# Kernel tuning notes

Hardware: AMD Instinct MI355X
Metric: run time of the kernel (lower is better)

Reference implementation:

```python
import jax, jax.numpy as jnp
import numpy as np


def setup_inputs() -> dict:
    key = jax.random.key(0)
    k1, k2 = jax.random.split(key)
    D = 512
    B, N = 32, 512
    panel_embeddings = jax.random.normal(k1, (B, N, D), dtype=jnp.float32)
    # nn.Bilinear(D, D, 1) weight: (1, D, D) -> squeeze to (D, D); bias: scalar
    bound = 1.0 / np.sqrt(D)
    W = jax.random.uniform(k2, (D, D), dtype=jnp.float32, minval=-bound, maxval=bound)
    b = jnp.float32(0.0)
    return {"panel_embeddings": panel_embeddings, "W": W, "b": b}


def reference(panel_embeddings, W, b):
    # score[b,i,j] = x_i^T W x_j + b, with diagonal forced to 0 (loop skips i==j)
    xw = jnp.einsum('bid,de->bie', panel_embeddings, W)          # (B, N, D)
    scores = jnp.einsum('bie,bje->bij', xw, panel_embeddings) + b  # (B, N, N)
    N = panel_embeddings.shape[1]
    mask = ~jnp.eye(N, dtype=bool)
    return jnp.where(mask, scores, jnp.zeros_like(scores))
```

## Files before the change

### kernel.cpp

```cpp
#include <hip/hip_runtime.h>
#include <stdint.h>

#define BATCH 32
#define NDIM 512
#define DDIM 512
#define XELEMS (BATCH * NDIM * DDIM)
#define WELEMS (DDIM * DDIM)

typedef _Float16 f16x8 __attribute__((ext_vector_type(8)));
typedef _Float16 f16x4v __attribute__((ext_vector_type(4)));
typedef float f32x4 __attribute__((ext_vector_type(4)));

__device__ __forceinline__ void gl_lds16(const _Float16* g, _Float16* l) {
    __builtin_amdgcn_global_load_lds(
        (const __attribute__((address_space(1))) unsigned int*)(g),
        (__attribute__((address_space(3))) unsigned int*)(l),
        16, 0, 0);
}

__global__ __launch_bounds__(256) void prep(const float4* __restrict__ X4,
                                            f16x4v* __restrict__ Xh4,
                                            const float* __restrict__ W,
                                            _Float16* __restrict__ Wt) {
    __shared__ float tile[32][33];
    int bid = blockIdx.x;
    if (bid < XELEMS / 4 / 256) {
        int i = bid * 256 + threadIdx.x;
        float4 v = X4[i];
        f16x4v o;
        o.x = (_Float16)v.x;
        o.y = (_Float16)v.y;
        o.z = (_Float16)v.z;
        o.w = (_Float16)v.w;
        Xh4[i] = o;
    } else {
        int t = bid - XELEMS / 4 / 256;
        int bx = t & 15;
        int by = t >> 4;
        int tx = threadIdx.x & 31;
        int ty = threadIdx.x >> 5;
        for (int r = ty; r < 32; r += 8)
            tile[r][tx] = W[(by * 32 + r) * DDIM + bx * 32 + tx];
        __syncthreads();
        for (int r = ty; r < 32; r += 8)
            Wt[(size_t)(bx * 32 + r) * DDIM + by * 32 + tx] = (_Float16)tile[tx][r];
    }
}

__global__ __launch_bounds__(512) void fused(const _Float16* __restrict__ Xh,
                                             const _Float16* __restrict__ Wt,
                                             float* __restrict__ Sout,
                                             const float* __restrict__ bias_ptr) {
    __shared__ __align__(16) _Float16 Ylds[64 * 512];
    __shared__ __align__(16) _Float16 As[8 * 512];
    __shared__ __align__(16) _Float16 Bs[64 * 512];

    const int tid  = threadIdx.x;
    const int lane = tid & 63;
    const int wv   = tid >> 6;
    const int quad = lane >> 4;
    const int l16  = lane & 15;

    const int lr = lane >> 3;
    const int lc = lane & 7;
    const int lk = (lc ^ lr) * 8;

    const int blk   = blockIdx.x;
    const int batch = blk & 31;
    const int r0    = (blk >> 5) * 64;

    const _Float16* Xb = Xh + (size_t)batch * (NDIM * DDIM);

    f32x4 acc[4][4];
#pragma unroll
    for (int i = 0; i < 4; ++i)
#pragma unroll
        for (int j = 0; j < 4; ++j)
            acc[i][j] = (f32x4){0.f, 0.f, 0.f, 0.f};

    for (int it = 0; it < 8; ++it) {
        const int k0 = it * 64;
        gl_lds16(Xb + (size_t)(r0 + wv * 8 + lr) * DDIM + k0 + lk, &As[wv * 512]);
#pragma unroll
        for (int t = 0; t < 8; ++t)
            gl_lds16(Wt + (size_t)(wv * 64 + t * 8 + lr) * DDIM + k0 + lk,
                     &Bs[(wv * 8 + t) * 512]);
        __syncthreads();

#pragma unroll
        for (int kkc = 0; kkc < 8; kkc += 4) {
            const int pa = (((kkc + quad) ^ (l16 & 7)) * 8);
            f16x8 a[4], b[4];
#pragma unroll
            for (int mt = 0; mt < 4; ++mt)
                a[mt] = *(const f16x8*)&As[(mt * 16 + l16) * 64 + pa];
#pragma unroll
            for (int nt = 0; nt < 4; ++nt)
                b[nt] = *(const f16x8*)&Bs[(wv * 64 + nt * 16 + l16) * 64 + pa];
#pragma unroll
            for (int mt = 0; mt < 4; ++mt)
#pragma unroll
                for (int nt = 0; nt < 4; ++nt)
                    acc[mt][nt] = __builtin_amdgcn_mfma_f32_16x16x32_f16(
                        a[mt], b[nt], acc[mt][nt], 0, 0, 0);
        }
        __syncthreads();
    }

#pragma unroll
    for (int mt = 0; mt < 4; ++mt)
#pragma unroll
        for (int nt = 0; nt < 4; ++nt)
#pragma unroll
            for (int r = 0; r < 4; ++r) {
                int i = mt * 16 + quad * 4 + r;
                int e = wv * 64 + nt * 16 + l16;
                int c = e >> 3, j = e & 7;
                Ylds[i * 512 + (((c ^ (i & 7)) << 3) | j)] = (_Float16)acc[mt][nt][r];
            }
    __syncthreads();

#pragma unroll
    for (int i = 0; i < 4; ++i)
#pragma unroll
        for (int j = 0; j < 4; ++j)
            acc[i][j] = (f32x4){0.f, 0.f, 0.f, 0.f};

    for (int it = 0; it < 8; ++it) {
        const int e0 = it * 64;
#pragma unroll
        for (int t = 0; t < 8; ++t)
            gl_lds16(Xb + (size_t)(wv * 64 + t * 8 + lr) * DDIM + e0 + lk,
                     &Bs[(wv * 8 + t) * 512]);
        __syncthreads();

#pragma unroll
        for (int kkc = 0; kkc < 8; kkc += 4) {
            const int pa = (((kkc + quad) ^ (l16 & 7)) * 8);
            const int cy = it * 8 + kkc + quad;
            const int pay = ((cy ^ (l16 & 7)) * 8);
            f16x8 a[4], b[4];
#pragma unroll
            for (int mt = 0; mt < 4; ++mt)
                a[mt] = *(const f16x8*)&Ylds[(mt * 16 + l16) * 512 + pay];
#pragma unroll
            for (int nt = 0; nt < 4; ++nt)
                b[nt] = *(const f16x8*)&Bs[(wv * 64 + nt * 16 + l16) * 64 + pa];
#pragma unroll
            for (int mt = 0; mt < 4; ++mt)
#pragma unroll
                for (int nt = 0; nt < 4; ++nt)
                    acc[mt][nt] = __builtin_amdgcn_mfma_f32_16x16x32_f16(
                        a[mt], b[nt], acc[mt][nt], 0, 0, 0);
        }
        __syncthreads();
    }

    const float bias = bias_ptr[0];
#pragma unroll
    for (int mt = 0; mt < 4; ++mt)
#pragma unroll
        for (int nt = 0; nt < 4; ++nt)
#pragma unroll
            for (int r = 0; r < 4; ++r) {
                int gi = r0 + mt * 16 + quad * 4 + r;
                int gj = wv * 64 + nt * 16 + l16;
                float v = acc[mt][nt][r] + bias;
                if (gi == gj) v = 0.f;
                Sout[((size_t)batch * NDIM + gi) * NDIM + gj] = v;
            }
}

extern "C" void kernel_launch(void* const* d_in, const int* in_sizes, int n_in,
                              void* d_out, int out_size, void* d_ws, size_t ws_size,
                              hipStream_t stream) {
    const float* X  = (const float*)d_in[0];
    const float* W  = (const float*)d_in[1];
    const float* bp = (const float*)d_in[2];
    float* out = (float*)d_out;

    _Float16* Xh = (_Float16*)d_ws;
    _Float16* Wt = Xh + XELEMS;

    prep<<<XELEMS / 4 / 256 + 256, 256, 0, stream>>>((const float4*)X, (f16x4v*)Xh, W, Wt);

    fused<<<256, 512, 0, stream>>>(Xh, Wt, out, bp);

    (void)in_sizes; (void)n_in; (void)out_size; (void)ws_size;
}
```

Baseline: 114.4 us.

## Double-buffer LDS tiles with K=32 steps to overlap global loads and MFMA

Replaces the single-buffered 64-wide K tiles with two 32-wide LDS buffers, so the next tile's global-to-LDS loads are issued before the current tile's MFMAs run. One barrier per iteration is removed. The last iteration of the first GEMM also prefetches the first X tile for the second GEMM. LDS footprint stays about the same, but iteration count doubles and the swizzle changes.

```diff
diff --git a/kernel.cpp b/kernel.cpp
--- a/kernel.cpp
+++ b/kernel.cpp
@@ -52,8 +52,8 @@
                                              float* __restrict__ Sout,
                                              const float* __restrict__ bias_ptr) {
     __shared__ __align__(16) _Float16 Ylds[64 * 512];
-    __shared__ __align__(16) _Float16 As[8 * 512];
-    __shared__ __align__(16) _Float16 Bs[64 * 512];
+    __shared__ __align__(16) _Float16 As2[2][64 * 32];
+    __shared__ __align__(16) _Float16 Bs2[2][512 * 32];
 
     const int tid  = threadIdx.x;
     const int lane = tid & 63;
@@ -61,9 +61,11 @@
     const int quad = lane >> 4;
     const int l16  = lane & 15;
 
-    const int lr = lane >> 3;
-    const int lc = lane & 7;
-    const int lk = (lc ^ lr) * 8;
+    const int lr2 = lane >> 2;
+    const int lc2 = lane & 3;
+    const int lk2 = (lc2 ^ ((lr2 >> 1) & 3)) * 8;
+
+    const int paK = (quad ^ ((l16 >> 1) & 3)) * 8;
 
     const int blk   = blockIdx.x;
     const int batch = blk & 31;
@@ -78,25 +80,45 @@
         for (int j = 0; j < 4; ++j)
             acc[i][j] = (f32x4){0.f, 0.f, 0.f, 0.f};
 
-    for (int it = 0; it < 8; ++it) {
-        const int k0 = it * 64;
-        gl_lds16(Xb + (size_t)(r0 + wv * 8 + lr) * DDIM + k0 + lk, &As[wv * 512]);
-#pragma unroll
-        for (int t = 0; t < 8; ++t)
-            gl_lds16(Wt + (size_t)(wv * 64 + t * 8 + lr) * DDIM + k0 + lk,
-                     &Bs[(wv * 8 + t) * 512]);
-        __syncthreads();
-
-#pragma unroll
-        for (int kkc = 0; kkc < 8; kkc += 4) {
-            const int pa = (((kkc + quad) ^ (l16 & 7)) * 8);
+    if (wv < 4)
+        gl_lds16(Xb + (size_t)(r0 + wv * 16 + lr2) * DDIM + lk2, &As2[0][wv * 512]);
+#pragma unroll
+    for (int t = 0; t < 4; ++t) {
+        const int chunk = wv * 4 + t;
+        gl_lds16(Wt + (size_t)(chunk * 16 + lr2) * DDIM + lk2, &Bs2[0][chunk * 512]);
+    }
+    __syncthreads();
+
+    int buf = 0;
+    for (int it = 0; it < 16; ++it) {
+        if (it < 15) {
+            const int k0 = (it + 1) * 32;
+            if (wv < 4)
+                gl_lds16(Xb + (size_t)(r0 + wv * 16 + lr2) * DDIM + k0 + lk2,
+                         &As2[buf ^ 1][wv * 512]);
+#pragma unroll
+            for (int t = 0; t < 4; ++t) {
+                const int chunk = wv * 4 + t;
+                gl_lds16(Wt + (size_t)(chunk * 16 + lr2) * DDIM + k0 + lk2,
+                         &Bs2[buf ^ 1][chunk * 512]);
+            }
+        } else {
+#pragma unroll
+            for (int t = 0; t < 4; ++t) {
+                const int chunk = wv * 4 + t;
+                gl_lds16(Xb + (size_t)(chunk * 16 + lr2) * DDIM + lk2,
+                         &Bs2[buf ^ 1][chunk * 512]);
+            }
+        }
+
+        {
             f16x8 a[4], b[4];
 #pragma unroll
             for (int mt = 0; mt < 4; ++mt)
-                a[mt] = *(const f16x8*)&As[(mt * 16 + l16) * 64 + pa];
+                a[mt] = *(const f16x8*)&As2[buf][(mt * 16 + l16) * 32 + paK];
 #pragma unroll
             for (int nt = 0; nt < 4; ++nt)
-                b[nt] = *(const f16x8*)&Bs[(wv * 64 + nt * 16 + l16) * 64 + pa];
+                b[nt] = *(const f16x8*)&Bs2[buf][(wv * 64 + nt * 16 + l16) * 32 + paK];
 #pragma unroll
             for (int mt = 0; mt < 4; ++mt)
 #pragma unroll
@@ -105,6 +127,7 @@
                         a[mt], b[nt], acc[mt][nt], 0, 0, 0);
         }
         __syncthreads();
+        buf ^= 1;
     }
 
 #pragma unroll
@@ -126,26 +149,26 @@
         for (int j = 0; j < 4; ++j)
             acc[i][j] = (f32x4){0.f, 0.f, 0.f, 0.f};
 
-    for (int it = 0; it < 8; ++it) {
-        const int e0 = it * 64;
-#pragma unroll
-        for (int t = 0; t < 8; ++t)
-            gl_lds16(Xb + (size_t)(wv * 64 + t * 8 + lr) * DDIM + e0 + lk,
-                     &Bs[(wv * 8 + t) * 512]);
-        __syncthreads();
-
-#pragma unroll
-        for (int kkc = 0; kkc < 8; kkc += 4) {
-            const int pa = (((kkc + quad) ^ (l16 & 7)) * 8);
-            const int cy = it * 8 + kkc + quad;
-            const int pay = ((cy ^ (l16 & 7)) * 8);
+    for (int it = 0; it < 16; ++it) {
+        if (it < 15) {
+            const int e0 = (it + 1) * 32;
+#pragma unroll
+            for (int t = 0; t < 4; ++t) {
+                const int chunk = wv * 4 + t;
+                gl_lds16(Xb + (size_t)(chunk * 16 + lr2) * DDIM + e0 + lk2,
+                         &Bs2[buf ^ 1][chunk * 512]);
+            }
+        }
+
+        {
+            const int pay = (((it * 4 + quad) ^ (l16 & 7)) * 8);
             f16x8 a[4], b[4];
 #pragma unroll
             for (int mt = 0; mt < 4; ++mt)
                 a[mt] = *(const f16x8*)&Ylds[(mt * 16 + l16) * 512 + pay];
 #pragma unroll
             for (int nt = 0; nt < 4; ++nt)
-                b[nt] = *(const f16x8*)&Bs[(wv * 64 + nt * 16 + l16) * 64 + pa];
+                b[nt] = *(const f16x8*)&Bs2[buf][(wv * 64 + nt * 16 + l16) * 32 + paK];
 #pragma unroll
             for (int mt = 0; mt < 4; ++mt)
 #pragma unroll
@@ -154,6 +177,7 @@
                         a[mt], b[nt], acc[mt][nt], 0, 0, 0);
         }
         __syncthreads();
+        buf ^= 1;
     }
 
     const float bias = bias_ptr[0];
```

New measurement: 120.7 us. 5.5% more time.

## Double-buffer per-wave LDS tiles with vmcnt waits instead of block barriers

Applied to the files above, without the earlier changes.

Restructures both GEMM phases of the fused kernel. The whole 64x512 X row block now loads into LDS up front, and each wave double-buffers its own B tiles in 32-wide K steps. Explicit s_waitcnt vmcnt replaces per-iteration __syncthreads, since each wave only reads data it loaded itself. Phase-2 data is prefetched across the phase boundary, and LDS is shrunk by merging the A and Y buffers. The aim is to overlap global-to-LDS loads with MFMA work and remove block-wide barrier stalls, at the cost of fragile hand-managed wait counts and a new swizzle.

```diff
diff --git a/kernel.cpp b/kernel.cpp
--- a/kernel.cpp
+++ b/kernel.cpp
@@ -17,6 +17,9 @@
         (__attribute__((address_space(3))) unsigned int*)(l),
         16, 0, 0);
 }
+
+#define WAITVM(N) do { asm volatile("s_waitcnt vmcnt(" #N ")" ::: "memory"); \
+                       __builtin_amdgcn_sched_barrier(0); } while (0)
 
 __global__ __launch_bounds__(256) void prep(const float4* __restrict__ X4,
                                             f16x4v* __restrict__ Xh4,
@@ -51,9 +54,8 @@
                                              const _Float16* __restrict__ Wt,
                                              float* __restrict__ Sout,
                                              const float* __restrict__ bias_ptr) {
-    __shared__ __align__(16) _Float16 Ylds[64 * 512];
-    __shared__ __align__(16) _Float16 As[8 * 512];
-    __shared__ __align__(16) _Float16 Bs[64 * 512];
+    __shared__ __align__(16) _Float16 AY[64 * 512];
+    __shared__ __align__(16) _Float16 Bs[2][8 * 2048];
 
     const int tid  = threadIdx.x;
     const int lane = tid & 63;
@@ -61,9 +63,11 @@
     const int quad = lane >> 4;
     const int l16  = lane & 15;
 
-    const int lr = lane >> 3;
-    const int lc = lane & 7;
-    const int lk = (lc ^ lr) * 8;
+    const int lr2 = lane >> 2;
+    const int lc2 = lane & 3;
+    const int lk2 = (lc2 ^ ((lr2 >> 1) & 3)) * 8;
+
+    const int paK = (quad ^ ((l16 >> 1) & 3)) * 8;
 
     const int blk   = blockIdx.x;
     const int batch = blk & 31;
@@ -78,35 +82,66 @@
         for (int j = 0; j < 4; ++j)
             acc[i][j] = (f32x4){0.f, 0.f, 0.f, 0.f};
 
-    for (int it = 0; it < 8; ++it) {
-        const int k0 = it * 64;
-        gl_lds16(Xb + (size_t)(r0 + wv * 8 + lr) * DDIM + k0 + lk, &As[wv * 512]);
-#pragma unroll
-        for (int t = 0; t < 8; ++t)
-            gl_lds16(Wt + (size_t)(wv * 64 + t * 8 + lr) * DDIM + k0 + lk,
-                     &Bs[(wv * 8 + t) * 512]);
-        __syncthreads();
-
-#pragma unroll
-        for (int kkc = 0; kkc < 8; kkc += 4) {
-            const int pa = (((kkc + quad) ^ (l16 & 7)) * 8);
-            f16x8 a[4], b[4];
-#pragma unroll
-            for (int mt = 0; mt < 4; ++mt)
-                a[mt] = *(const f16x8*)&As[(mt * 16 + l16) * 64 + pa];
-#pragma unroll
-            for (int nt = 0; nt < 4; ++nt)
-                b[nt] = *(const f16x8*)&Bs[(wv * 64 + nt * 16 + l16) * 64 + pa];
-#pragma unroll
-            for (int mt = 0; mt < 4; ++mt)
-#pragma unroll
-                for (int nt = 0; nt < 4; ++nt)
-                    acc[mt][nt] = __builtin_amdgcn_mfma_f32_16x16x32_f16(
-                        a[mt], b[nt], acc[mt][nt], 0, 0, 0);
-        }
-        __syncthreads();
-    }
-
+#pragma unroll
+    for (int c = 0; c < 8; ++c) {
+        const int kt = wv * 2 + (c >> 2);
+        const int rc = c & 3;
+        gl_lds16(Xb + (size_t)(r0 + rc * 16 + lr2) * DDIM + kt * 32 + lk2,
+                 &AY[(kt * 4 + rc) * 512]);
+    }
+#pragma unroll
+    for (int t = 0; t < 4; ++t)
+        gl_lds16(Wt + (size_t)(wv * 64 + t * 16 + lr2) * DDIM + lk2,
+                 &Bs[0][wv * 2048 + t * 512]);
+    WAITVM(4);
+    __builtin_amdgcn_s_barrier();
+
+#pragma unroll
+    for (int it = 0; it < 15; ++it) {
+        const int buf = it & 1;
+        const int k0 = (it + 1) * 32;
+#pragma unroll
+        for (int t = 0; t < 4; ++t)
+            gl_lds16(Wt + (size_t)(wv * 64 + t * 16 + lr2) * DDIM + k0 + lk2,
+                     &Bs[buf ^ 1][wv * 2048 + t * 512]);
+        WAITVM(4);
+        f16x8 a[4], b[4];
+#pragma unroll
+        for (int mt = 0; mt < 4; ++mt)
+            a[mt] = *(const f16x8*)&AY[(it * 4 + mt) * 512 + l16 * 32 + paK];
+#pragma unroll
+        for (int nt = 0; nt < 4; ++nt)
+            b[nt] = *(const f16x8*)&Bs[buf][wv * 2048 + nt * 512 + l16 * 32 + paK];
+#pragma unroll
+        for (int mt = 0; mt < 4; ++mt)
+#pragma unroll
+            for (int nt = 0; nt < 4; ++nt)
+                acc[mt][nt] = __builtin_amdgcn_mfma_f32_16x16x32_f16(
+                    a[mt], b[nt], acc[mt][nt], 0, 0, 0);
+    }
+    {
+        const int buf = 15 & 1;
+#pragma unroll
+        for (int t = 0; t < 4; ++t)
+            gl_lds16(Xb + (size_t)(wv * 64 + t * 16 + lr2) * DDIM + lk2,
+                     &Bs[buf ^ 1][wv * 2048 + t * 512]);
+        WAITVM(4);
+        f16x8 a[4], b[4];
+#pragma unroll
+        for (int mt = 0; mt < 4; ++mt)
+            a[mt] = *(const f16x8*)&AY[(15 * 4 + mt) * 512 + l16 * 32 + paK];
+#pragma unroll
+        for (int nt = 0; nt < 4; ++nt)
+            b[nt] = *(const f16x8*)&Bs[buf][wv * 2048 + nt * 512 + l16 * 32 + paK];
+#pragma unroll
+        for (int mt = 0; mt < 4; ++mt)
+#pragma unroll
+            for (int nt = 0; nt < 4; ++nt)
+                acc[mt][nt] = __builtin_amdgcn_mfma_f32_16x16x32_f16(
+                    a[mt], b[nt], acc[mt][nt], 0, 0, 0);
+    }
+
+    __builtin_amdgcn_s_barrier();
 #pragma unroll
     for (int mt = 0; mt < 4; ++mt)
 #pragma unroll
@@ -116,9 +151,10 @@
                 int i = mt * 16 + quad * 4 + r;
                 int e = wv * 64 + nt * 16 + l16;
                 int c = e >> 3, j = e & 7;
-                Ylds[i * 512 + (((c ^ (i & 7)) << 3) | j)] = (_Float16)acc[mt][nt][r];
+                AY[i * 512 + (((c ^ (i & 7)) << 3) | j)] = (_Float16)acc[mt][nt][r];
             }
-    __syncthreads();
+    asm volatile("s_waitcnt lgkmcnt(0)" ::: "memory");
+    __builtin_amdgcn_s_barrier();
 
 #pragma unroll
     for (int i = 0; i < 4; ++i)
@@ -126,34 +162,47 @@
         for (int j = 0; j < 4; ++j)
             acc[i][j] = (f32x4){0.f, 0.f, 0.f, 0.f};
 
-    for (int it = 0; it < 8; ++it) {
-        const int e0 = it * 64;
-#pragma unroll
-        for (int t = 0; t < 8; ++t)
-            gl_lds16(Xb + (size_t)(wv * 64 + t * 8 + lr) * DDIM + e0 + lk,
-                     &Bs[(wv * 8 + t) * 512]);
-        __syncthreads();
-
-#pragma unroll
-        for (int kkc = 0; kkc < 8; kkc += 4) {
-            const int pa = (((kkc + quad) ^ (l16 & 7)) * 8);
-            const int cy = it * 8 + kkc + quad;
-            const int pay = ((cy ^ (l16 & 7)) * 8);
-            f16x8 a[4], b[4];
-#pragma unroll
-            for (int mt = 0; mt < 4; ++mt)
-                a[mt] = *(const f16x8*)&Ylds[(mt * 16 + l16) * 512 + pay];
-#pragma unroll
-            for (int nt = 0; nt < 4; ++nt)
-                b[nt] = *(const f16x8*)&Bs[(wv * 64 + nt * 16 + l16) * 64 + pa];
-#pragma unroll
-            for (int mt = 0; mt < 4; ++mt)
-#pragma unroll
-                for (int nt = 0; nt < 4; ++nt)
-                    acc[mt][nt] = __builtin_amdgcn_mfma_f32_16x16x32_f16(
-                        a[mt], b[nt], acc[mt][nt], 0, 0, 0);
-        }
-        __syncthreads();
+#pragma unroll
+    for (int it = 0; it < 15; ++it) {
+        const int buf = it & 1;
+        const int e0 = (it + 1) * 32;
+#pragma unroll
+        for (int t = 0; t < 4; ++t)
+            gl_lds16(Xb + (size_t)(wv * 64 + t * 16 + lr2) * DDIM + e0 + lk2,
+                     &Bs[buf ^ 1][wv * 2048 + t * 512]);
+        WAITVM(4);
+        const int pay = (((it * 4 + quad) ^ (l16 & 7)) * 8);
+        f16x8 a[4], b[4];
+#pragma unroll
+        for (int mt = 0; mt < 4; ++mt)
+            a[mt] = *(const f16x8*)&AY[(mt * 16 + l16) * 512 + pay];
+#pragma unroll
+        for (int nt = 0; nt < 4; ++nt)
+            b[nt] = *(const f16x8*)&Bs[buf][wv * 2048 + nt * 512 + l16 * 32 + paK];
+#pragma unroll
+        for (int mt = 0; mt < 4; ++mt)
+#pragma unroll
+            for (int nt = 0; nt < 4; ++nt)
+                acc[mt][nt] = __builtin_amdgcn_mfma_f32_16x16x32_f16(
+                    a[mt], b[nt], acc[mt][nt], 0, 0, 0);
+    }
+    {
+        const int buf = 15 & 1;
+        WAITVM(0);
+        const int pay = (((15 * 4 + quad) ^ (l16 & 7)) * 8);
+        f16x8 a[4], b[4];
+#pragma unroll
+        for (int mt = 0; mt < 4; ++mt)
+            a[mt] = *(const f16x8*)&AY[(mt * 16 + l16) * 512 + pay];
+#pragma unroll
+        for (int nt = 0; nt < 4; ++nt)
+            b[nt] = *(const f16x8*)&Bs[buf][wv * 2048 + nt * 512 + l16 * 32 + paK];
+#pragma unroll
+        for (int mt = 0; mt < 4; ++mt)
+#pragma unroll
+            for (int nt = 0; nt < 4; ++nt)
+                acc[mt][nt] = __builtin_amdgcn_mfma_f32_16x16x32_f16(
+                    a[mt], b[nt], acc[mt][nt], 0, 0, 0);
     }
 
     const float bias = bias_ptr[0];
```

After: 110.0 us. 1.04x faster.
